# Optimization experiments

Measured on AMD Instinct MI355X. Metric: run time of the kernel, lower is better.

The kernel has to match this reference:

```python
import jax, jax.numpy as jnp
import numpy as np

N, S, IN_F, TEXT_D, EMB, H = 128, 1024, 768, 512, 512, 8
HD = EMB // H  # 64


def setup_inputs() -> dict:
    key = jax.random.key(0)
    ks = jax.random.split(key, 14)
    sc = 0.02
    return {
        "v": jax.random.normal(ks[0], (1, N, 12, IN_F), dtype=jnp.float32),
        "t": jax.random.normal(ks[1], (N, S, TEXT_D), dtype=jnp.float32),
        "t_len": jax.random.randint(ks[2], (N,), 1, S + 1, dtype=jnp.int32),
        "W_fc1": jax.random.normal(ks[3], (EMB, IN_F), dtype=jnp.float32) * sc,
        "b_fc1": jnp.zeros((EMB,), jnp.float32),
        "W_fc2": jax.random.normal(ks[4], (EMB, 12 * EMB), dtype=jnp.float32) * sc,
        "b_fc2": jnp.zeros((EMB,), jnp.float32),
        "Wq": jax.random.normal(ks[5], (EMB, EMB), dtype=jnp.float32) * sc,
        "Wk": jax.random.normal(ks[6], (EMB, TEXT_D), dtype=jnp.float32) * sc,
        "Wv": jax.random.normal(ks[7], (EMB, TEXT_D), dtype=jnp.float32) * sc,
        "bq": jnp.zeros((EMB,), jnp.float32),
        "bk": jnp.zeros((EMB,), jnp.float32),
        "bv": jnp.zeros((EMB,), jnp.float32),
        "Wo": jax.random.normal(ks[8], (EMB, EMB), dtype=jnp.float32) * sc,
        "bo": jnp.zeros((EMB,), jnp.float32),
    }


def reference(v, t, t_len, W_fc1, b_fc1, W_fc2, b_fc2, Wq, Wk, Wv, bq, bk, bv, Wo, bo):
    # fc1 + ReLU: [1,N,12,IN_F] -> [N,12,EMB]
    x = jax.nn.relu(jnp.einsum('onif,ef->onie', v, W_fc1) + b_fc1)[0]
    # flatten + fc2 + ReLU -> [N, EMB]
    x = x.reshape(N, 12 * EMB)
    vfeat = jax.nn.relu(x @ W_fc2.T + b_fc2)
    # Batched ragged multihead attention, query length 1 per item.
    scale = 1.0 / jnp.sqrt(jnp.asarray(HD, vfeat.dtype))
    q = ((vfeat @ Wq.T + bq) * scale).reshape(N, H, HD)           # [N,H,HD]
    k = (jnp.einsum('nsd,ed->nse', t, Wk) + bk).reshape(N, S, H, HD)
    vv = (jnp.einsum('nsd,ed->nse', t, Wv) + bv).reshape(N, S, H, HD)
    scores = jnp.einsum('nhd,nshd->nhs', q, k)                    # [N,H,S]
    valid = (jnp.arange(S)[None, :] < t_len[:, None])[:, None, :]  # [N,1,S]
    scores = jnp.where(valid, scores, jnp.finfo(scores.dtype).min)
    w = jax.nn.softmax(scores, axis=-1)                           # [N,H,S]
    ctx = jnp.einsum('nhs,nshd->nhd', w, vv).reshape(N, EMB)
    attn_out = ctx @ Wo.T + bo                                    # [N,EMB]
    return vfeat, attn_out
```

## Files before the change

### kernel.cpp

```cpp
#include <hip/hip_runtime.h>

#define NB 128
#define SSEQ 1024
#define TD 512

typedef _Float16 half8 __attribute__((ext_vector_type(8)));
typedef _Float16 half4 __attribute__((ext_vector_type(4)));
typedef float f32x4 __attribute__((ext_vector_type(4)));

template<int AM, int BM>
__global__ __launch_bounds__(256) void k_gemm(
    const void* __restrict__ Av, int lda, long aSZ,
    const void* __restrict__ Bv, int ldb, long bSZ,
    const float* __restrict__ bias, const float* __restrict__ aRowScale,
    float scale, int doRelu, int outMode,
    float* __restrict__ outF, _Float16* __restrict__ outH,
    int ldc, int cColOff, int mtiles, int kTiles, long oSplit)
{
  __shared__ _Float16 As[64][72];
  __shared__ _Float16 Bs[64][72];
  int mt = blockIdx.x % mtiles, nt = blockIdx.x / mtiles;
  int sp = blockIdx.y, bz = blockIdx.z;
  int tid = threadIdx.x;
  int r = tid >> 2, kq = (tid & 3) * 16;
  int w = tid >> 6, l = tid & 63;
  long aoff = (long)bz * aSZ + (long)(mt * 64 + r) * lda + (long)sp * kTiles * 64 + kq;
  long boff = (long)bz * bSZ + (long)(nt * 64 + r) * ldb + (long)sp * kTiles * 64 + kq;
  const _Float16* apH = (const _Float16*)Av + aoff;
  const float*    apF = (const float*)Av + aoff;
  const _Float16* bpH = (const _Float16*)Bv + boff;
  const float*    bpF = (const float*)Bv + boff;
  float srA = 1.0f;
  if constexpr (AM == 2) srA = 1.0f / aRowScale[(mt * 64 + r) * 8 + bz];

  half8 pa0, pa1, pb0, pb1;
  f32x4 qa0, qa1, qa2, qa3, qc0, qc1, qc2, qc3;
  if constexpr (AM == 0) { pa0 = *(const half8*)apH; pa1 = *(const half8*)(apH + 8); }
  else { qa0 = *(const f32x4*)apF; qa1 = *(const f32x4*)(apF + 4);
         qa2 = *(const f32x4*)(apF + 8); qa3 = *(const f32x4*)(apF + 12); }
  if constexpr (BM == 0) { pb0 = *(const half8*)bpH; pb1 = *(const half8*)(bpH + 8); }
  else { qc0 = *(const f32x4*)bpF; qc1 = *(const f32x4*)(bpF + 4);
         qc2 = *(const f32x4*)(bpF + 8); qc3 = *(const f32x4*)(bpF + 12); }

  f32x4 acc[4];
  #pragma unroll
  for (int c = 0; c < 4; ++c) acc[c] = (f32x4){0.f, 0.f, 0.f, 0.f};
  int fr = l & 15, fo = (l >> 4) * 8;
  for (int kt = 0; kt < kTiles; ++kt) {
    __syncthreads();
    if constexpr (AM == 0) {
      *(half8*)&As[r][kq] = pa0; *(half8*)&As[r][kq + 8] = pa1;
    } else {
      f32x4 s0 = qa0, s1 = qa1, s2 = qa2, s3 = qa3;
      if constexpr (AM == 2) { s0 *= srA; s1 *= srA; s2 *= srA; s3 *= srA; }
      *(half4*)&As[r][kq + 0]  = __builtin_convertvector(s0, half4);
      *(half4*)&As[r][kq + 4]  = __builtin_convertvector(s1, half4);
      *(half4*)&As[r][kq + 8]  = __builtin_convertvector(s2, half4);
      *(half4*)&As[r][kq + 12] = __builtin_convertvector(s3, half4);
    }
    if constexpr (BM == 0) {
      *(half8*)&Bs[r][kq] = pb0; *(half8*)&Bs[r][kq + 8] = pb1;
    } else {
      *(half4*)&Bs[r][kq + 0]  = __builtin_convertvector(qc0, half4);
      *(half4*)&Bs[r][kq + 4]  = __builtin_convertvector(qc1, half4);
      *(half4*)&Bs[r][kq + 8]  = __builtin_convertvector(qc2, half4);
      *(half4*)&Bs[r][kq + 12] = __builtin_convertvector(qc3, half4);
    }
    __syncthreads();
    if (kt + 1 < kTiles) {
      apH += 64; apF += 64; bpH += 64; bpF += 64;
      if constexpr (AM == 0) { pa0 = *(const half8*)apH; pa1 = *(const half8*)(apH + 8); }
      else { qa0 = *(const f32x4*)apF; qa1 = *(const f32x4*)(apF + 4);
             qa2 = *(const f32x4*)(apF + 8); qa3 = *(const f32x4*)(apF + 12); }
      if constexpr (BM == 0) { pb0 = *(const half8*)bpH; pb1 = *(const half8*)(bpH + 8); }
      else { qc0 = *(const f32x4*)bpF; qc1 = *(const f32x4*)(bpF + 4);
             qc2 = *(const f32x4*)(bpF + 8); qc3 = *(const f32x4*)(bpF + 12); }
    }
    #pragma unroll
    for (int ks = 0; ks < 2; ++ks) {
      half8 af = *(const half8*)&As[16 * w + fr][ks * 32 + fo];
      #pragma unroll
      for (int c = 0; c < 4; ++c) {
        half8 bf = *(const half8*)&Bs[16 * c + fr][ks * 32 + fo];
        acc[c] = __builtin_amdgcn_mfma_f32_16x16x32_f16(af, bf, acc[c], 0, 0, 0);
      }
    }
  }
  int lrow = (l >> 4) * 4, lcol = l & 15;
  #pragma unroll
  for (int c = 0; c < 4; ++c) {
    #pragma unroll
    for (int rr = 0; rr < 4; ++rr) {
      int gm = mt * 64 + 16 * w + lrow + rr;
      int gn = nt * 64 + 16 * c + lcol;
      int ecol = gn + bz * cColOff;
      float vv = acc[c][rr];
      if (bias) vv += bias[ecol];
      vv *= scale;
      if (doRelu) vv = fmaxf(vv, 0.f);
      long oidx = (long)gm * ldc + ecol;
      if (outMode == 0) outF[oidx] = vv;
      else if (outMode == 1) outH[oidx] = (_Float16)vv;
      else outF[oidx + (long)sp * oSplit] = vv;
    }
  }
}

__global__ __launch_bounds__(256) void k_prep(
    const float* __restrict__ Wq, const float* __restrict__ Wk,
    const float* __restrict__ bq, const float* __restrict__ bk,
    _Float16* __restrict__ G16T, float* __restrict__ gb,
    float* __restrict__ qbc, float* __restrict__ cvec,
    float* __restrict__ pz, _Float16* __restrict__ qz)
{
  int b = blockIdx.x, tid = threadIdx.x;
  int gid = b * 256 + tid;
  for (long i = gid; i < 131328; i += 131072)
    *(f32x4*)(pz + 4 * i) = (f32x4){0.f, 0.f, 0.f, 0.f};
  {
    long i4 = (long)gid * 4;
    long n = i4 >> 12, off = i4 & 4095;
    *(half4*)(qz + n * 8192 + 4096 + off) = (half4){(_Float16)0, (_Float16)0, (_Float16)0, (_Float16)0};
  }
  int h = b >> 6, et = (b >> 3) & 7, dt = b & 7;
  __shared__ float Aq[64][68];
  __shared__ float Bk[64][68];
  __shared__ float bqs[64], bks[64];
  int r = tid >> 2, cq = (tid & 3) * 16;
  const float* wqp = Wq + (long)(h * 64 + r) * 512 + et * 64 + cq;
  const float* wkp = Wk + (long)(h * 64 + r) * 512 + dt * 64 + cq;
  #pragma unroll
  for (int c = 0; c < 4; ++c) {
    *(f32x4*)&Aq[r][cq + 4 * c] = *(const f32x4*)(wqp + 4 * c);
    *(f32x4*)&Bk[r][cq + 4 * c] = *(const f32x4*)(wkp + 4 * c);
  }
  if (tid < 64) { bqs[tid] = bq[h * 64 + tid]; bks[tid] = bk[h * 64 + tid]; }
  __syncthreads();
  int te = tid & 15, td = tid >> 4;
  float acc[4][4];
  #pragma unroll
  for (int a = 0; a < 4; ++a)
    #pragma unroll
    for (int d = 0; d < 4; ++d) acc[a][d] = 0.f;
  #pragma unroll 4
  for (int j = 0; j < 64; ++j) {
    f32x4 av = *(const f32x4*)&Aq[j][te * 4];
    f32x4 bv = *(const f32x4*)&Bk[j][td * 4];
    #pragma unroll
    for (int a = 0; a < 4; ++a)
      #pragma unroll
      for (int d = 0; d < 4; ++d) acc[a][d] = fmaf(av[a], bv[d], acc[a][d]);
  }
  #pragma unroll
  for (int d = 0; d < 4; ++d) {
    half4 hv = { (_Float16)(0.125f * acc[0][d]), (_Float16)(0.125f * acc[1][d]),
                 (_Float16)(0.125f * acc[2][d]), (_Float16)(0.125f * acc[3][d]) };
    *(half4*)(G16T + (long)h * 262144 + (long)(dt * 64 + td * 4 + d) * 512 + et * 64 + te * 4) = hv;
  }
  if (dt == 0 && td == 0) {
    #pragma unroll
    for (int i = 0; i < 4; ++i) {
      float s = 0.f;
      for (int j = 0; j < 64; ++j) s = fmaf(Aq[j][te * 4 + i], bks[j], s);
      gb[h * 512 + et * 64 + te * 4 + i] = 0.125f * s;
    }
  }
  if (et == 0 && te == 0) {
    #pragma unroll
    for (int i = 0; i < 4; ++i) {
      float s = 0.f;
      for (int j = 0; j < 64; ++j) s = fmaf(Bk[j][td * 4 + i], bqs[j], s);
      cvec[h * 512 + dt * 64 + td * 4 + i] = 0.125f * s;
    }
  }
  if (et == 0 && dt == 0 && tid == 0) {
    float s = 0.f;
    for (int j = 0; j < 64; ++j) s = fmaf(bqs[j], bks[j], s);
    qbc[h] = 0.125f * s;
  }
}

__global__ __launch_bounds__(256) void k_vfeat(
    const float* __restrict__ vacc, const float* __restrict__ b2,
    float* __restrict__ outF, _Float16* __restrict__ vf16)
{
  int i = blockIdx.x * 256 + threadIdx.x;
  float vv = b2[i & 511];
  #pragma unroll
  for (int sp = 0; sp < 16; ++sp) vv += vacc[sp * 65536 + i];
  vv = fmaxf(vv, 0.f);
  outF[i] = vv;
  vf16[i] = (_Float16)vv;
}

__global__ __launch_bounds__(256) void k_qb(
    const _Float16* __restrict__ vf16, const float* __restrict__ gb,
    const float* __restrict__ qbc, float* __restrict__ qb)
{
  int n = blockIdx.x, tid = threadIdx.x;
  __shared__ float qs[512];
  qs[tid] = (float)vf16[n * 512 + tid];
  qs[tid + 256] = (float)vf16[n * 512 + tid + 256];
  __syncthreads();
  int h = tid >> 5, j = tid & 31;
  float p = 0.f;
  for (int e = j; e < 512; e += 32) p = fmaf(qs[e], gb[h * 512 + e], p);
  #pragma unroll
  for (int m = 1; m < 32; m <<= 1) p += __shfl_xor(p, m, 32);
  if (j == 0) qb[n * 8 + h] = p + qbc[h];
}

__global__ __launch_bounds__(256) void k_attn(
    const float* __restrict__ t, const int* __restrict__ tlen,
    const _Float16* __restrict__ qk16, const float* __restrict__ qb,
    float* __restrict__ pu, float* __restrict__ pl)
{
  int n = blockIdx.x >> 4, j = blockIdx.x & 15;
  int len = tlen[n];
  int base0 = j * 64;
  if (base0 >= len) return;
  int tid = threadIdx.x, wid = tid >> 6, l = tid & 63;
  int fr = l & 15, fo = (l >> 4) * 8;

  __shared__ __align__(16) _Float16 ts[32][520];
  __shared__ __align__(16) _Float16 wst[16][32];
  __shared__ float lred[8];
  if (tid < 8) lred[tid] = 0.f;

  const float* tn = t + (long)n * SSEQ * TD;
  const _Float16* qn = qk16 + (long)n * 8192 + fr * 512 + fo;
  float qbr = (fr < 8) ? qb[n * 8 + fr] : 0.f;

  f32x4 upv[8];
  #pragma unroll
  for (int dt = 0; dt < 8; ++dt) upv[dt] = (f32x4){0.f, 0.f, 0.f, 0.f};

  #pragma unroll 1
  for (int sub = 0; sub < 2; ++sub) {
    int base = base0 + sub * 32;
    if (base >= len) break;
    int s1 = base + 32; if (s1 > len) s1 = len;
    __syncthreads();
    {
      f32x4 a0, a1, b0, b1;
      auto ld = [&](int c, f32x4& x0, f32x4& x1) {
        int sg = base + c * 4 + wid;
        if (sg < s1) {
          const float* p = tn + (long)sg * TD;
          x0 = *(const f32x4*)(p + 4 * l);
          x1 = *(const f32x4*)(p + 256 + 4 * l);
        } else {
          x0 = (f32x4){0.f,0.f,0.f,0.f}; x1 = (f32x4){0.f,0.f,0.f,0.f};
        }
      };
      ld(0, a0, a1); ld(1, b0, b1);
      #pragma unroll
      for (int c = 0; c < 8; c += 2) {
        half4 h0 = __builtin_convertvector(a0, half4);
        half4 h1 = __builtin_convertvector(a1, half4);
        int row = c * 4 + wid;
        if (c + 2 < 8) ld(c + 2, a0, a1);
        *(half4*)&ts[row][4 * l] = h0;
        *(half4*)&ts[row][256 + 4 * l] = h1;
        half4 g0 = __builtin_convertvector(b0, half4);
        half4 g1 = __builtin_convertvector(b1, half4);
        int row2 = c * 4 + 4 + wid;
        if (c + 3 < 8) ld(c + 3, b0, b1);
        *(half4*)&ts[row2][4 * l] = g0;
        *(half4*)&ts[row2][256 + 4 * l] = g1;
      }
    }
    __syncthreads();
    if (wid < 2) {
      f32x4 acc = (f32x4){0.f, 0.f, 0.f, 0.f};
      #pragma unroll 4
      for (int kt = 0; kt < 16; ++kt) {
        half8 bf = *(const half8*)(qn + kt * 32);
        half8 af = *(const half8*)&ts[16 * wid + fr][kt * 32 + fo];
        acc = __builtin_amdgcn_mfma_f32_16x16x32_f16(af, bf, acc, 0, 0, 0);
      }
      float lac = 0.f;
      #pragma unroll
      for (int r = 0; r < 4; ++r) {
        int sl = 16 * wid + (l >> 4) * 4 + r;
        float wv = (fr < 8 && base + sl < s1) ? __expf(acc[r] + qbr) : 0.f;
        wst[fr][sl] = (_Float16)wv;
        lac += wv;
      }
      if (fr < 8) atomicAdd(&lred[fr], lac);
    }
    __syncthreads();
    {
      half8 af = *(const half8*)&wst[fr][fo];
      #pragma unroll
      for (int dt = 0; dt < 8; ++dt) {
        int dcol = 128 * wid + dt * 16 + fr;
        half8 bf;
        #pragma unroll
        for (int jj = 0; jj < 8; ++jj) bf[jj] = ts[fo + jj][dcol];
        upv[dt] = __builtin_amdgcn_mfma_f32_16x16x32_f16(af, bf, upv[dt], 0, 0, 0);
      }
    }
  }
  int quad = l >> 4;
  float* pn = pu + (long)n * 4096;
  if (quad < 2) {
    #pragma unroll
    for (int dt = 0; dt < 8; ++dt) {
      int d = 128 * wid + dt * 16 + fr;
      #pragma unroll
      for (int r = 0; r < 4; ++r)
        atomicAdd(&pn[(quad * 4 + r) * 512 + d], upv[dt][r]);
    }
  }
  if (tid < 8) atomicAdd(&pl[n * 8 + tid], lred[tid]);
}

extern "C" void kernel_launch(void* const* d_in, const int* in_sizes, int n_in,
                              void* d_out, int out_size, void* d_ws, size_t ws_size,
                              hipStream_t stream)
{
  const float* v    = (const float*)d_in[0];
  const float* t    = (const float*)d_in[1];
  const int*   tlen = (const int*)d_in[2];
  const float* W1   = (const float*)d_in[3];
  const float* b1   = (const float*)d_in[4];
  const float* W2   = (const float*)d_in[5];
  const float* b2   = (const float*)d_in[6];
  const float* Wq   = (const float*)d_in[7];
  const float* Wk   = (const float*)d_in[8];
  const float* Wv   = (const float*)d_in[9];
  const float* bq   = (const float*)d_in[10];
  const float* bk   = (const float*)d_in[11];
  const float* bv   = (const float*)d_in[12];
  const float* Wo   = (const float*)d_in[13];
  const float* bo   = (const float*)d_in[14];
  float* out = (float*)d_out;

  _Float16* hb   = (_Float16*)d_ws;
  _Float16* x16  = hb;
  _Float16* vf16 = hb + 786432l;
  _Float16* ctx16= hb + 851968l;
  _Float16* qk16 = hb + 917504l;
  _Float16* G16T = hb + 1966080l;
  float* fb   = (float*)(hb + 4063232l);
  float* vacc = fb;
  float* pu   = fb + 1048576l;
  float* pl   = fb + 1572864l;
  float* qb   = fb + 1573888l;
  float* gb   = fb + 1574912l;
  float* qbc  = fb + 1579008l;
  float* cvec = fb + 1579024l;

  k_prep<<<512, 256, 0, stream>>>(Wq, Wk, bq, bk, G16T, gb, qbc, cvec, pu, qk16);
  k_gemm<1,1><<<dim3(192, 1, 1), 256, 0, stream>>>(v, 768, 0, W1, 768, 0,
      b1, nullptr, 1.f, 1, 1, nullptr, x16, 512, 0, 24, 12, 0);
  k_gemm<0,1><<<dim3(16, 16, 1), 256, 0, stream>>>(x16, 6144, 0, W2, 6144, 0,
      nullptr, nullptr, 1.f, 0, 2, vacc, nullptr, 512, 0, 2, 6, 65536);
  k_vfeat<<<256, 256, 0, stream>>>(vacc, b2, out, vf16);
  k_gemm<0,0><<<dim3(16, 1, 8), 256, 0, stream>>>(vf16, 512, 0, G16T, 512, 262144,
      cvec, nullptr, 1.f, 0, 1, nullptr, qk16, 8192, 512, 2, 8, 0);
  k_qb<<<128, 256, 0, stream>>>(vf16, gb, qbc, qb);
  k_attn<<<NB * 16, 256, 0, stream>>>(t, tlen, qk16, qb, pu, pl);
  k_gemm<2,1><<<dim3(2, 1, 8), 256, 0, stream>>>(pu, 4096, 512, Wv, 512, 32768,
      bv, pl, 1.f, 0, 1, nullptr, ctx16, 512, 64, 2, 8, 0);
  k_gemm<0,1><<<dim3(16, 1, 1), 256, 0, stream>>>(ctx16, 512, 0, Wo, 512, 0,
      bo, nullptr, 1.f, 0, 0, out + 65536, nullptr, 512, 0, 2, 8, 0);
}
```

Before: 464.7 us.

## Merge independent launches and process 64-row attention tiles in one pass

Folds the fc1 GEMM into the weight-prep kernel and the qk GEMM into the qb kernel, using block-index dispatch so each pair shares one launch and two fewer launches remain. The attention kernel now stages all 64 sequence rows at once, with a 516-element row stride, and has all four waves compute scores instead of looping over two 32-row halves where only two waves did the score MFMAs. This is meant to cut launch overhead, barriers and idle waves. In exchange it uses more shared memory per block, which may lower occupancy.

```diff
diff --git a/kernel.cpp b/kernel.cpp
--- a/kernel.cpp
+++ b/kernel.cpp
@@ -3,25 +3,24 @@
 #define NB 128
 #define SSEQ 1024
 #define TD 512
+#define TSTR 516
 
 typedef _Float16 half8 __attribute__((ext_vector_type(8)));
 typedef _Float16 half4 __attribute__((ext_vector_type(4)));
 typedef float f32x4 __attribute__((ext_vector_type(4)));
 
 template<int AM, int BM>
-__global__ __launch_bounds__(256) void k_gemm(
+__device__ __forceinline__ void gemm_body(
     const void* __restrict__ Av, int lda, long aSZ,
     const void* __restrict__ Bv, int ldb, long bSZ,
     const float* __restrict__ bias, const float* __restrict__ aRowScale,
     float scale, int doRelu, int outMode,
     float* __restrict__ outF, _Float16* __restrict__ outH,
-    int ldc, int cColOff, int mtiles, int kTiles, long oSplit)
+    int ldc, int cColOff, int kTiles, long oSplit,
+    int mt, int nt, int sp, int bz, int tid)
 {
   __shared__ _Float16 As[64][72];
   __shared__ _Float16 Bs[64][72];
-  int mt = blockIdx.x % mtiles, nt = blockIdx.x / mtiles;
-  int sp = blockIdx.y, bz = blockIdx.z;
-  int tid = threadIdx.x;
   int r = tid >> 2, kq = (tid & 3) * 16;
   int w = tid >> 6, l = tid & 63;
   long aoff = (long)bz * aSZ + (long)(mt * 64 + r) * lda + (long)sp * kTiles * 64 + kq;
@@ -106,14 +105,38 @@
   }
 }
 
-__global__ __launch_bounds__(256) void k_prep(
+template<int AM, int BM>
+__global__ __launch_bounds__(256) void k_gemm(
+    const void* __restrict__ Av, int lda, long aSZ,
+    const void* __restrict__ Bv, int ldb, long bSZ,
+    const float* __restrict__ bias, const float* __restrict__ aRowScale,
+    float scale, int doRelu, int outMode,
+    float* __restrict__ outF, _Float16* __restrict__ outH,
+    int ldc, int cColOff, int mtiles, int kTiles, long oSplit)
+{
+  gemm_body<AM, BM>(Av, lda, aSZ, Bv, ldb, bSZ, bias, aRowScale, scale, doRelu,
+                    outMode, outF, outH, ldc, cColOff, kTiles, oSplit,
+                    (int)blockIdx.x % mtiles, (int)blockIdx.x / mtiles,
+                    (int)blockIdx.y, (int)blockIdx.z, (int)threadIdx.x);
+}
+
+__global__ __launch_bounds__(256) void k_prepfc1(
     const float* __restrict__ Wq, const float* __restrict__ Wk,
     const float* __restrict__ bq, const float* __restrict__ bk,
     _Float16* __restrict__ G16T, float* __restrict__ gb,
     float* __restrict__ qbc, float* __restrict__ cvec,
-    float* __restrict__ pz, _Float16* __restrict__ qz)
-{
-  int b = blockIdx.x, tid = threadIdx.x;
+    float* __restrict__ pz, _Float16* __restrict__ qz,
+    const float* __restrict__ v, const float* __restrict__ W1,
+    const float* __restrict__ b1, _Float16* __restrict__ x16)
+{
+  int bx = blockIdx.x, tid = threadIdx.x;
+  if (bx >= 512) {
+    int s = bx - 512;
+    gemm_body<1, 1>(v, 768, 0, W1, 768, 0, b1, nullptr, 1.f, 1, 1,
+                    nullptr, x16, 512, 0, 12, 0, s % 24, s / 24, 0, 0, tid);
+    return;
+  }
+  int b = bx;
   int gid = b * 256 + tid;
   for (long i = gid; i < 131328; i += 131072)
     *(f32x4*)(pz + 4 * i) = (f32x4){0.f, 0.f, 0.f, 0.f};
@@ -193,11 +216,20 @@
   vf16[i] = (_Float16)vv;
 }
 
-__global__ __launch_bounds__(256) void k_qb(
-    const _Float16* __restrict__ vf16, const float* __restrict__ gb,
-    const float* __restrict__ qbc, float* __restrict__ qb)
-{
-  int n = blockIdx.x, tid = threadIdx.x;
+__global__ __launch_bounds__(256) void k_qkqb(
+    const _Float16* __restrict__ vf16, const _Float16* __restrict__ G16T,
+    const float* __restrict__ cvec, const float* __restrict__ gb,
+    const float* __restrict__ qbc, _Float16* __restrict__ qk16,
+    float* __restrict__ qb)
+{
+  int bx = blockIdx.x, tid = threadIdx.x;
+  if (bx < 128) {
+    int z = bx >> 4, s = bx & 15;
+    gemm_body<0, 0>(vf16, 512, 0, G16T, 512, 262144, cvec, nullptr, 1.f, 0, 1,
+                    nullptr, qk16, 8192, 512, 8, 0, s % 2, s / 2, 0, z, tid);
+    return;
+  }
+  int n = bx - 128;
   __shared__ float qs[512];
   qs[tid] = (float)vf16[n * 512 + tid];
   qs[tid + 256] = (float)vf16[n * 512 + tid + 256];
@@ -217,89 +249,85 @@
 {
   int n = blockIdx.x >> 4, j = blockIdx.x & 15;
   int len = tlen[n];
-  int base0 = j * 64;
-  if (base0 >= len) return;
+  int base = j * 64;
+  if (base >= len) return;
+  int s1 = base + 64; if (s1 > len) s1 = len;
   int tid = threadIdx.x, wid = tid >> 6, l = tid & 63;
   int fr = l & 15, fo = (l >> 4) * 8;
 
-  __shared__ __align__(16) _Float16 ts[32][520];
-  __shared__ __align__(16) _Float16 wst[16][32];
+  __shared__ __align__(16) _Float16 ts[64][TSTR];
+  __shared__ __align__(16) _Float16 wst[16][72];
   __shared__ float lred[8];
   if (tid < 8) lred[tid] = 0.f;
 
   const float* tn = t + (long)n * SSEQ * TD;
-  const _Float16* qn = qk16 + (long)n * 8192 + fr * 512 + fo;
-  float qbr = (fr < 8) ? qb[n * 8 + fr] : 0.f;
-
+  {
+    f32x4 a0, a1, b0, b1;
+    auto ld = [&](int c, f32x4& x0, f32x4& x1) {
+      int sg = base + c * 4 + wid;
+      if (sg < s1) {
+        const float* p = tn + (long)sg * TD;
+        x0 = *(const f32x4*)(p + 4 * l);
+        x1 = *(const f32x4*)(p + 256 + 4 * l);
+      } else {
+        x0 = (f32x4){0.f,0.f,0.f,0.f}; x1 = (f32x4){0.f,0.f,0.f,0.f};
+      }
+    };
+    ld(0, a0, a1); ld(1, b0, b1);
+    #pragma unroll
+    for (int c = 0; c < 16; c += 2) {
+      half4 h0 = __builtin_convertvector(a0, half4);
+      half4 h1 = __builtin_convertvector(a1, half4);
+      int row = c * 4 + wid;
+      if (c + 2 < 16) ld(c + 2, a0, a1);
+      *(half4*)&ts[row][4 * l] = h0;
+      *(half4*)&ts[row][256 + 4 * l] = h1;
+      half4 g0 = __builtin_convertvector(b0, half4);
+      half4 g1 = __builtin_convertvector(b1, half4);
+      int row2 = (c + 1) * 4 + wid;
+      if (c + 3 < 16) ld(c + 3, b0, b1);
+      *(half4*)&ts[row2][4 * l] = g0;
+      *(half4*)&ts[row2][256 + 4 * l] = g1;
+    }
+  }
+  __syncthreads();
+  {
+    const _Float16* qn = qk16 + (long)n * 8192 + fr * 512 + fo;
+    f32x4 acc = (f32x4){0.f, 0.f, 0.f, 0.f};
+    #pragma unroll 4
+    for (int kt = 0; kt < 16; ++kt) {
+      half8 bf = *(const half8*)(qn + kt * 32);
+      const _Float16* ap = &ts[16 * wid + fr][kt * 32 + fo];
+      half4 alo = *(const half4*)ap;
+      half4 ahi = *(const half4*)(ap + 4);
+      half8 af = { alo[0], alo[1], alo[2], alo[3], ahi[0], ahi[1], ahi[2], ahi[3] };
+      acc = __builtin_amdgcn_mfma_f32_16x16x32_f16(af, bf, acc, 0, 0, 0);
+    }
+    float qbr = (fr < 8) ? qb[n * 8 + fr] : 0.f;
+    float lac = 0.f;
+    #pragma unroll
+    for (int r = 0; r < 4; ++r) {
+      int sl = 16 * wid + (l >> 4) * 4 + r;
+      float wv = (fr < 8 && base + sl < s1) ? __expf(acc[r] + qbr) : 0.f;
+      wst[fr][sl] = (_Float16)wv;
+      lac += wv;
+    }
+    if (fr < 8) atomicAdd(&lred[fr], lac);
+  }
+  __syncthreads();
   f32x4 upv[8];
   #pragma unroll
   for (int dt = 0; dt < 8; ++dt) upv[dt] = (f32x4){0.f, 0.f, 0.f, 0.f};
-
-  #pragma unroll 1
-  for (int sub = 0; sub < 2; ++sub) {
-    int base = base0 + sub * 32;
-    if (base >= len) break;
-    int s1 = base + 32; if (s1 > len) s1 = len;
-    __syncthreads();
-    {
-      f32x4 a0, a1, b0, b1;
-      auto ld = [&](int c, f32x4& x0, f32x4& x1) {
-        int sg = base + c * 4 + wid;
-        if (sg < s1) {
-          const float* p = tn + (long)sg * TD;
-          x0 = *(const f32x4*)(p + 4 * l);
-          x1 = *(const f32x4*)(p + 256 + 4 * l);
-        } else {
-          x0 = (f32x4){0.f,0.f,0.f,0.f}; x1 = (f32x4){0.f,0.f,0.f,0.f};
-        }
-      };
-      ld(0, a0, a1); ld(1, b0, b1);
+  #pragma unroll
+  for (int dt = 0; dt < 8; ++dt) {
+    int dcol = 128 * wid + dt * 16 + fr;
+    #pragma unroll
+    for (int ks = 0; ks < 2; ++ks) {
+      half8 af = *(const half8*)&wst[fr][ks * 32 + fo];
+      half8 bf;
       #pragma unroll
-      for (int c = 0; c < 8; c += 2) {
-        half4 h0 = __builtin_convertvector(a0, half4);
-        half4 h1 = __builtin_convertvector(a1, half4);
-        int row = c * 4 + wid;
-        if (c + 2 < 8) ld(c + 2, a0, a1);
-        *(half4*)&ts[row][4 * l] = h0;
-        *(half4*)&ts[row][256 + 4 * l] = h1;
-        half4 g0 = __builtin_convertvector(b0, half4);
-        half4 g1 = __builtin_convertvector(b1, half4);
-        int row2 = c * 4 + 4 + wid;
-        if (c + 3 < 8) ld(c + 3, b0, b1);
-        *(half4*)&ts[row2][4 * l] = g0;
-        *(half4*)&ts[row2][256 + 4 * l] = g1;
-      }
-    }
-    __syncthreads();
-    if (wid < 2) {
-      f32x4 acc = (f32x4){0.f, 0.f, 0.f, 0.f};
-      #pragma unroll 4
-      for (int kt = 0; kt < 16; ++kt) {
-        half8 bf = *(const half8*)(qn + kt * 32);
-        half8 af = *(const half8*)&ts[16 * wid + fr][kt * 32 + fo];
-        acc = __builtin_amdgcn_mfma_f32_16x16x32_f16(af, bf, acc, 0, 0, 0);
-      }
-      float lac = 0.f;
-      #pragma unroll
-      for (int r = 0; r < 4; ++r) {
-        int sl = 16 * wid + (l >> 4) * 4 + r;
-        float wv = (fr < 8 && base + sl < s1) ? __expf(acc[r] + qbr) : 0.f;
-        wst[fr][sl] = (_Float16)wv;
-        lac += wv;
-      }
-      if (fr < 8) atomicAdd(&lred[fr], lac);
-    }
-    __syncthreads();
-    {
-      half8 af = *(const half8*)&wst[fr][fo];
-      #pragma unroll
-      for (int dt = 0; dt < 8; ++dt) {
-        int dcol = 128 * wid + dt * 16 + fr;
-        half8 bf;
-        #pragma unroll
-        for (int jj = 0; jj < 8; ++jj) bf[jj] = ts[fo + jj][dcol];
-        upv[dt] = __builtin_amdgcn_mfma_f32_16x16x32_f16(af, bf, upv[dt], 0, 0, 0);
-      }
+      for (int jj = 0; jj < 8; ++jj) bf[jj] = ts[ks * 32 + fo + jj][dcol];
+      upv[dt] = __builtin_amdgcn_mfma_f32_16x16x32_f16(af, bf, upv[dt], 0, 0, 0);
     }
   }
   int quad = l >> 4;
@@ -352,15 +380,12 @@
   float* qbc  = fb + 1579008l;
   float* cvec = fb + 1579024l;
 
-  k_prep<<<512, 256, 0, stream>>>(Wq, Wk, bq, bk, G16T, gb, qbc, cvec, pu, qk16);
-  k_gemm<1,1><<<dim3(192, 1, 1), 256, 0, stream>>>(v, 768, 0, W1, 768, 0,
-      b1, nullptr, 1.f, 1, 1, nullptr, x16, 512, 0, 24, 12, 0);
+  k_prepfc1<<<704, 256, 0, stream>>>(Wq, Wk, bq, bk, G16T, gb, qbc, cvec,
+                                     pu, qk16, v, W1, b1, x16);
   k_gemm<0,1><<<dim3(16, 16, 1), 256, 0, stream>>>(x16, 6144, 0, W2, 6144, 0,
       nullptr, nullptr, 1.f, 0, 2, vacc, nullptr, 512, 0, 2, 6, 65536);
   k_vfeat<<<256, 256, 0, stream>>>(vacc, b2, out, vf16);
-  k_gemm<0,0><<<dim3(16, 1, 8), 256, 0, stream>>>(vf16, 512, 0, G16T, 512, 262144,
-      cvec, nullptr, 1.f, 0, 1, nullptr, qk16, 8192, 512, 2, 8, 0);
-  k_qb<<<128, 256, 0, stream>>>(vf16, gb, qbc, qb);
+  k_qkqb<<<256, 256, 0, stream>>>(vf16, G16T, cvec, gb, qbc, qk16, qb);
   k_attn<<<NB * 16, 256, 0, stream>>>(t, tlen, qk16, qb, pu, pl);
   k_gemm<2,1><<<dim3(2, 1, 8), 256, 0, stream>>>(pu, 4096, 512, Wv, 512, 32768,
       bv, pl, 1.f, 0, 1, nullptr, ctx16, 512, 64, 2, 8, 0);
```

After: 464.5 us. Within noise of the previous version (-0.1%).
